# Optimization experiments

Hardware: AMD Instinct MI355X
Metric: run time of the kernel (lower is better)

Reference implementation:

```python
import jax, jax.numpy as jnp
import numpy as np

EPS = 1e-8

def _fft_unit_proj(x):
    # Project each vector to unit magnitude in the Fourier domain (norm_kv=True).
    f = jnp.fft.fft(x, axis=-1)
    return jnp.real(jnp.fft.ifft(f / (jnp.abs(f) + EPS), axis=-1))

def _hrr_key_value_query(k, v, q, causal=True):
    # k, v, q: [B, S, D]
    k = _fft_unit_proj(k)
    v = _fft_unit_proj(v)
    # bind: circular convolution of key and value
    kv = jnp.real(jnp.fft.ifft(jnp.fft.fft(k, axis=-1) * jnp.fft.fft(v, axis=-1), axis=-1))
    # causal associative memory: running sum of bound pairs along sequence
    if causal:
        mem = jnp.cumsum(kv, axis=1)
    else:
        mem = jnp.broadcast_to(jnp.sum(kv, axis=1, keepdims=True), kv.shape)
    # unbind: circular correlation of memory with query
    out = jnp.real(jnp.fft.ifft(jnp.conj(jnp.fft.fft(q, axis=-1)) * jnp.fft.fft(mem, axis=-1), axis=-1))
    return out


def setup_inputs() -> dict:
    key = jax.random.key(0)
    ks = jax.random.split(key, 8)
    B, S, D = 2, 4096, 2048
    sc = 1.0 / np.sqrt(D).astype(np.float32)
    return {
        "hidden_states": jax.random.normal(ks[0], (B, S, D), jnp.float32),
        "base_output": jax.random.normal(ks[1], (B, S, D), jnp.float32),
        "Wq": jax.random.normal(ks[2], (D, D), jnp.float32) * sc,
        "bq": jnp.zeros((D,), jnp.float32),
        "Wk": jax.random.normal(ks[3], (D, D), jnp.float32) * sc,
        "bk": jnp.zeros((D,), jnp.float32),
        "Wv": jax.random.normal(ks[4], (D, D), jnp.float32) * sc,
        "bv": jnp.zeros((D,), jnp.float32),
        "gate": jax.random.normal(ks[5], (1,), jnp.float32) * 0.1,
    }


def reference(hidden_states, base_output, Wq, bq, Wk, bk, Wv, bv, gate):
    # Adapter q/k/v projections (nn.Linear uses y = x @ W.T + b)
    q = jnp.einsum('bsd,ed->bse', hidden_states, Wq) + bq
    k = jnp.einsum('bsd,ed->bse', hidden_states, Wk) + bk
    v = jnp.einsum('bsd,ed->bse', hidden_states, Wv) + bv
    adapter = _hrr_key_value_query(k, v, q, causal=True)
    return base_output + gate * adapter
```

## Files before the change

kernel.cpp:

```cpp
#include <hip/hip_runtime.h>
#include <math.h>

constexpr int D_DIM  = 2048;
constexpr int HALF_D = 1024;
constexpr int B_DIM  = 2;
constexpr int S_DIM  = 4096;
constexpr int NROW   = B_DIM * S_DIM;
constexpr int NCHUNK = 64;
constexpr int CHLEN  = S_DIM / NCHUNK;
constexpr float EPS_ = 1e-8f;

typedef __attribute__((ext_vector_type(8))) short  short8;
typedef __attribute__((ext_vector_type(8))) unsigned short ushort8;
typedef __attribute__((ext_vector_type(4))) float  f32x4;

__device__ __forceinline__ float2 mkf2(float x, float y){ float2 r; r.x=x; r.y=y; return r; }
__device__ __forceinline__ float2 cmulf(float2 a, float2 b){
  return mkf2(fmaf(a.x, b.x, -a.y*b.y), fmaf(a.x, b.y, a.y*b.x));
}
__device__ __forceinline__ unsigned short f2bf(float x){
  unsigned u = __float_as_uint(x);
  u += 0x7fff + ((u >> 16) & 1);
  return (unsigned short)(u >> 16);
}
__device__ __forceinline__ float bf2f(unsigned short h){
  return __uint_as_float(((unsigned)h) << 16);
}

__global__ __launch_bounds__(256)
void cvt_f32_bf16(const float* __restrict__ in, unsigned short* __restrict__ out, int n8)
{
  int i = blockIdx.x * 256 + threadIdx.x;
  if (i >= n8) return;
  const float4* p = (const float4*)in + (size_t)i * 2;
  float4 a = p[0], b = p[1];
  ushort8 o;
  o[0]=f2bf(a.x); o[1]=f2bf(a.y); o[2]=f2bf(a.z); o[3]=f2bf(a.w);
  o[4]=f2bf(b.x); o[5]=f2bf(b.y); o[6]=f2bf(b.z); o[7]=f2bf(b.w);
  *(ushort8*)(out + (size_t)i * 8) = o;
}

__global__ __launch_bounds__(512, 2)
void gemm_fused(const unsigned short* __restrict__ A,
                const unsigned short* __restrict__ Wc,
                const float* __restrict__ bq, const float* __restrict__ bk,
                const float* __restrict__ bv,
                float* __restrict__ qout, float* __restrict__ kout,
                unsigned short* __restrict__ vout)
{
  constexpr int K = 2048, NT = K / 32;
  __shared__ unsigned short lds[49152];
  const int tid  = threadIdx.x;
  const int wid  = tid >> 6, lane = tid & 63;
  const int wr   = wid >> 2, wc = wid & 3;

  int bid = blockIdx.x;
  int sw  = (bid & 7) * 96 + (bid >> 3);
  const int bm = (sw / 24) * 256, bn = (sw % 24) * 256;

  const int srow = tid >> 2;
  const int skc  = ((tid & 3) ^ ((tid >> 3) & 3)) * 8;
  const unsigned short* Ag = A  + (size_t)(bm + srow) * K + skc;
  const unsigned short* Bg = Wc + (size_t)(bn + srow) * K + skc;

  unsigned short* Abase = lds;
  unsigned short* Bbase = lds + 24576;
  const int stoff = wid * 512;

  const int fr  = lane & 15;
  const int sig = ((lane >> 4) ^ ((lane >> 1) & 3)) * 8;
  const int aro = (wr * 128 + fr) * 32 + sig;
  const int bro = (wc * 64 + fr) * 32 + sig;

  auto stA = [&](int kt, int b, int r) {
    __builtin_amdgcn_global_load_lds(
      (const __attribute__((address_space(1))) void*)(Ag + (size_t)r * 128 * K + kt * 32),
      (__attribute__((address_space(3))) void*)(Abase + b * 8192 + r * 4096 + stoff),
      16, 0, 0);
  };
  auto stB = [&](int kt, int b, int r) {
    __builtin_amdgcn_global_load_lds(
      (const __attribute__((address_space(1))) void*)(Bg + (size_t)r * 128 * K + kt * 32),
      (__attribute__((address_space(3))) void*)(Bbase + b * 8192 + r * 4096 + stoff),
      16, 0, 0);
  };

  f32x4 acc[8][4];
#pragma unroll
  for (int i = 0; i < 8; ++i)
#pragma unroll
    for (int j = 0; j < 4; ++j) acc[i][j] = (f32x4){0.f, 0.f, 0.f, 0.f};

  stA(0, 0, 0); stA(0, 0, 1); stB(0, 0, 0); stB(0, 0, 1);
  stA(1, 1, 0); stA(1, 1, 1); stB(1, 1, 0); stB(1, 1, 1);
  asm volatile("s_waitcnt vmcnt(4)" ::: "memory");
  __builtin_amdgcn_s_barrier();
  __builtin_amdgcn_sched_barrier(0);

  int c = 0;
#pragma unroll 1
  for (int kt = 0; kt < NT; ++kt) {
    const unsigned short* Ab = Abase + c * 8192;
    const unsigned short* Bb = Bbase + c * 8192;
    int nb = c + 2; if (nb >= 3) nb -= 3;

    if (kt < NT - 2) { stA(kt + 2, nb, 0); stA(kt + 2, nb, 1); }
    short8 af0[4], bfr[4];
#pragma unroll
    for (int i = 0; i < 4; ++i) af0[i] = *(const short8*)(Ab + aro + i * 512);
#pragma unroll
    for (int j = 0; j < 4; ++j) bfr[j] = *(const short8*)(Bb + bro + j * 512);
    __builtin_amdgcn_s_setprio(1);
#pragma unroll
    for (int i = 0; i < 4; ++i)
#pragma unroll
      for (int j = 0; j < 4; ++j)
        acc[i][j] = __builtin_amdgcn_mfma_f32_16x16x32_bf16(af0[i], bfr[j], acc[i][j], 0, 0, 0);
    __builtin_amdgcn_s_setprio(0);

    if (kt < NT - 2) { stB(kt + 2, nb, 0); stB(kt + 2, nb, 1); }
    short8 af1[4];
#pragma unroll
    for (int i = 0; i < 4; ++i) af1[i] = *(const short8*)(Ab + aro + 2048 + i * 512);
    __builtin_amdgcn_s_setprio(1);
#pragma unroll
    for (int i = 0; i < 4; ++i)
#pragma unroll
      for (int j = 0; j < 4; ++j)
        acc[4 + i][j] = __builtin_amdgcn_mfma_f32_16x16x32_bf16(af1[i], bfr[j], acc[4 + i][j], 0, 0, 0);
    __builtin_amdgcn_s_setprio(0);

    if (kt < NT - 1) {
      if (kt < NT - 2) asm volatile("s_waitcnt vmcnt(4)" ::: "memory");
      else             asm volatile("s_waitcnt vmcnt(0)" ::: "memory");
      __builtin_amdgcn_s_barrier();
      __builtin_amdgcn_sched_barrier(0);
    }
    c = (c == 2) ? 0 : c + 1;
  }

  const int seg = bn >> 11;
  const float* bp = (seg == 0) ? bq : (seg == 1) ? bk : bv;
  float bias_j[4];
#pragma unroll
  for (int j = 0; j < 4; ++j)
    bias_j[j] = bp[(bn + wc * 64 + j * 16 + fr) & 2047];
  const int er = (lane >> 4) * 4;
#pragma unroll
  for (int I = 0; I < 8; ++I) {
    int row = bm + wr * 128 + (I >> 2) * 64 + (I & 3) * 16 + er;
#pragma unroll
    for (int j = 0; j < 4; ++j) {
      int col = (bn + wc * 64 + j * 16 + fr) & 2047;
#pragma unroll
      for (int r = 0; r < 4; ++r) {
        float val = acc[I][j][r] + bias_j[j];
        if (seg == 2)
          vout[(size_t)(row + r) * 2048 + col] = f2bf(val);
        else if (seg == 1)
          kout[(size_t)(row + r) * 2048 + col] = val;
        else
          qout[(size_t)(row + r) * 2048 + col] = val;
      }
    }
  }
}

__device__ __forceinline__ int XS(int i){ return i ^ (((i >> 5) ^ (i >> 10)) & 31); }
__device__ __forceinline__ int TS(int i){ return i ^ ((i >> 5) & 31); }

__device__ __forceinline__ float2 mulmi(float2 w){ return mkf2(w.y, -w.x); }
__device__ __forceinline__ float2 mulw8(float2 w){
  const float c = 0.70710678118654752f;
  return mkf2(c * (w.x + w.y), c * (w.y - w.x));
}
__device__ __forceinline__ void bfly(float2& a, float2& b, float2 w){
  float2 v = cmulf(w, b);
  b = mkf2(a.x - v.x, a.y - v.y);
  a = mkf2(a.x + v.x, a.y + v.y);
}
__device__ __forceinline__ void bflyc(float2& a, float2& b, float2 w){
  float2 d = mkf2(a.x - b.x, a.y - b.y);
  a = mkf2(a.x + b.x, a.y + b.y);
  b = mkf2(fmaf(d.x, w.x, d.y * w.y), fmaf(d.y, w.x, -d.x * w.y));
}

__device__ __forceinline__ void fwd8(float2 e[8], float2 wA, float2 wB0, float2 wC0){
  bfly(e[0], e[1], wA); bfly(e[2], e[3], wA); bfly(e[4], e[5], wA); bfly(e[6], e[7], wA);
  float2 wB1 = mulmi(wB0);
  bfly(e[0], e[2], wB0); bfly(e[1], e[3], wB1); bfly(e[4], e[6], wB0); bfly(e[5], e[7], wB1);
  float2 wC1 = mulw8(wC0), wC2 = mulmi(wC0), wC3 = mulmi(wC1);
  bfly(e[0], e[4], wC0); bfly(e[1], e[5], wC1); bfly(e[2], e[6], wC2); bfly(e[3], e[7], wC3);
}
__device__ __forceinline__ void inv8(float2 e[8], float2 wA, float2 wB0, float2 wC0){
  float2 wC1 = mulw8(wC0), wC2 = mulmi(wC0), wC3 = mulmi(wC1);
  bflyc(e[0], e[4], wC0); bflyc(e[1], e[5], wC1); bflyc(e[2], e[6], wC2); bflyc(e[3], e[7], wC3);
  float2 wB1 = mulmi(wB0);
  bflyc(e[0], e[2], wB0); bflyc(e[1], e[3], wB1); bflyc(e[4], e[6], wB0); bflyc(e[5], e[7], wB1);
  bflyc(e[0], e[1], wA); bflyc(e[2], e[3], wA); bflyc(e[4], e[5], wA); bflyc(e[6], e[7], wA);
}

__device__ __forceinline__ float2 twld(const float* twr, const float* twi, int i){
  int s = TS(i);
  return mkf2(twr[s], twi[s]);
}

__device__ void fft_fwd(float2* X, const float* twr, const float* twi, int t)
{
  const float2 one = mkf2(1.f, 0.f);
  {
    int b = 8 * t;
    float2 e[8];
#pragma unroll
    for (int r = 0; r < 8; ++r) e[r] = X[XS(b + r)];
    fwd8(e, one, one, one);
#pragma unroll
    for (int r = 0; r < 8; ++r) X[XS(b + r)] = e[r];
  }
  __syncthreads();
  {
    int u = t >> 5, b = 64 * (t & 31) + u;
    float2 e[8];
#pragma unroll
    for (int r = 0; r < 8; ++r) e[r] = X[XS(b + 8 * r)];
    fwd8(e, twld(twr,twi,128*u), twld(twr,twi,64*u), twld(twr,twi,32*u));
#pragma unroll
    for (int r = 0; r < 8; ++r) X[XS(b + 8 * r)] = e[r];
  }
  __syncthreads();
  {
    int u = t & 63, b = 512 * (t >> 6) + u;
    float2 e[8];
#pragma unroll
    for (int r = 0; r < 8; ++r) e[r] = X[XS(b + 64 * r)];
    fwd8(e, twld(twr,twi,16*u), twld(twr,twi,8*u), twld(twr,twi,4*u));
#pragma unroll
    for (int r = 0; r < 8; ++r) X[XS(b + 64 * r)] = e[r];
  }
  __syncthreads();
#pragma unroll
  for (int h = 0; h < 2; ++h) {
    int u = t + 256 * h;
    float2 f[4];
#pragma unroll
    for (int r = 0; r < 4; ++r) f[r] = X[XS(u + 512 * r)];
    float2 wA = twld(twr,twi,2*u), wB0 = twld(twr,twi,u), wB1 = mulmi(wB0);
    bfly(f[0], f[1], wA);  bfly(f[2], f[3], wA);
    bfly(f[0], f[2], wB0); bfly(f[1], f[3], wB1);
#pragma unroll
    for (int r = 0; r < 4; ++r) X[XS(u + 512 * r)] = f[r];
  }
  __syncthreads();
}

__device__ void fft_inv(float2* X, const float* twr, const float* twi, int t)
{
  const float2 one = mkf2(1.f, 0.f);
#pragma unroll
  for (int h = 0; h < 2; ++h) {
    int u = t + 256 * h;
    float2 f[4];
#pragma unroll
    for (int r = 0; r < 4; ++r) f[r] = X[XS(u + 512 * r)];
    float2 wA = twld(twr,twi,2*u), wB0 = twld(twr,twi,u), wB1 = mulmi(wB0);
    bflyc(f[0], f[2], wB0); bflyc(f[1], f[3], wB1);
    bflyc(f[0], f[1], wA);  bflyc(f[2], f[3], wA);
#pragma unroll
    for (int r = 0; r < 4; ++r) X[XS(u + 512 * r)] = f[r];
  }
  __syncthreads();
  {
    int u = t & 63, b = 512 * (t >> 6) + u;
    float2 e[8];
#pragma unroll
    for (int r = 0; r < 8; ++r) e[r] = X[XS(b + 64 * r)];
    inv8(e, twld(twr,twi,16*u), twld(twr,twi,8*u), twld(twr,twi,4*u));
#pragma unroll
    for (int r = 0; r < 8; ++r) X[XS(b + 64 * r)] = e[r];
  }
  __syncthreads();
  {
    int u = t >> 5, b = 64 * (t & 31) + u;
    float2 e[8];
#pragma unroll
    for (int r = 0; r < 8; ++r) e[r] = X[XS(b + 8 * r)];
    inv8(e, twld(twr,twi,128*u), twld(twr,twi,64*u), twld(twr,twi,32*u));
#pragma unroll
    for (int r = 0; r < 8; ++r) X[XS(b + 8 * r)] = e[r];
  }
  __syncthreads();
  {
    int b = 8 * t;
    float2 e[8];
#pragma unroll
    for (int r = 0; r < 8; ++r) e[r] = X[XS(b + r)];
    inv8(e, one, one, one);
#pragma unroll
    for (int r = 0; r < 8; ++r) X[XS(b + r)] = e[r];
  }
  __syncthreads();
}

__global__ __launch_bounds__(256)
void twiddle_init(float2* __restrict__ twg)
{
  int i = blockIdx.x * 256 + threadIdx.x;
  if (i < HALF_D) {
    float sv, cv;
    sincosf(-6.283185307179586f * (float)i / (float)D_DIM, &sv, &cv);
    twg[i] = mkf2(cv, sv);
  }
}

__global__ __launch_bounds__(256)
void fftkv_kernel(float* __restrict__ kbuf, const unsigned short* __restrict__ vbuf,
                  const float2* __restrict__ twg)
{
  __shared__ float2 X[D_DIM];
  __shared__ float twr[HALF_D], twi[HALF_D];
  const int t = threadIdx.x;
  const size_t row = blockIdx.x;
  const float* krow = kbuf + row * D_DIM;
  const unsigned short* vrow = vbuf + row * D_DIM;

  for (int i = t; i < HALF_D; i += 256) {
    float2 w = twg[i]; int s = TS(i); twr[s] = w.x; twi[s] = w.y;
  }
  for (int i = t; i < D_DIM; i += 256) {
    int p = __brev((unsigned)i) >> 21;
    X[XS(p)] = mkf2(krow[i], bf2f(vrow[i]));
  }
  __syncthreads();
  fft_fwd(X, twr, twi, t);

  float2* outp = (float2*)(kbuf + row * D_DIM);
  for (int d = t; d < HALF_D; d += 256) {
    float2 p;
    if (d == 0) {
      float2 z0 = X[XS(0)], zn = X[XS(HALF_D)];
      float k0 = z0.x, v0 = z0.y, kn = zn.x, vn = zn.y;
      float p0 = (k0 / (fabsf(k0) + EPS_)) * (v0 / (fabsf(v0) + EPS_));
      float pn = (kn / (fabsf(kn) + EPS_)) * (vn / (fabsf(vn) + EPS_));
      p = mkf2(p0, pn);
    } else {
      float2 A = X[XS(d)];
      float2 Bc = X[XS(D_DIM - d)];
      float2 Bj = mkf2(Bc.x, -Bc.y);
      float2 Fk = mkf2(0.5f * (A.x + Bj.x), 0.5f * (A.y + Bj.y));
      float2 tt = mkf2(0.5f * (A.x - Bj.x), 0.5f * (A.y - Bj.y));
      float2 Fv = mkf2(tt.y, -tt.x);
      float sa = 1.f / (sqrtf(Fk.x*Fk.x + Fk.y*Fk.y) + EPS_);
      float sb = 1.f / (sqrtf(Fv.x*Fv.x + Fv.y*Fv.y) + EPS_);
      p = cmulf(Fk, Fv);
      float sc = sa * sb;
      p.x *= sc; p.y *= sc;
    }
    outp[d] = p;
  }
}

__global__ __launch_bounds__(256)
void scan_partial(const float2* __restrict__ kv, float2* __restrict__ part)
{
  int gid = blockIdx.x * 256 + threadIdx.x;
  int d = gid & (HALF_D - 1);
  int chunk = (gid >> 10) & (NCHUNK - 1);
  int b = gid >> 16;
  const float2* p = kv + ((size_t)(b * S_DIM + chunk * CHLEN) * HALF_D) + d;
  float2 acc = mkf2(0.f, 0.f);
  for (int s = 0; s < CHLEN; ++s) {
    float2 v = p[(size_t)s * HALF_D];
    acc.x += v.x; acc.y += v.y;
  }
  part[gid] = acc;
}

__global__ __launch_bounds__(256)
void scan_offsets(float2* __restrict__ part)
{
  int gid = blockIdx.x * 256 + threadIdx.x;
  int d = gid & (HALF_D - 1);
  int b = gid >> 10;
  float2* p = part + (size_t)b * (NCHUNK * HALF_D) + d;
  float2 acc = mkf2(0.f, 0.f);
  for (int c = 0; c < NCHUNK; ++c) {
    float2 v = p[(size_t)c * HALF_D];
    p[(size_t)c * HALF_D] = acc;
    acc.x += v.x; acc.y += v.y;
  }
}

__global__ __launch_bounds__(256)
void scan_apply(float2* __restrict__ kv, const float2* __restrict__ part)
{
  int gid = blockIdx.x * 256 + threadIdx.x;
  int d = gid & (HALF_D - 1);
  int chunk = (gid >> 10) & (NCHUNK - 1);
  int b = gid >> 16;
  float2* p = kv + ((size_t)(b * S_DIM + chunk * CHLEN) * HALF_D) + d;
  float2 acc = part[gid];
  for (int s = 0; s < CHLEN; ++s) {
    float2 v = p[(size_t)s * HALF_D];
    acc.x += v.x; acc.y += v.y;
    p[(size_t)s * HALF_D] = acc;
  }
}

__global__ __launch_bounds__(256)
void final_kernel(float* __restrict__ qo, const float2* __restrict__ mem,
                  const float* __restrict__ base, const float* __restrict__ gate,
                  const float2* __restrict__ twg)
{
  __shared__ float2 X[D_DIM];
  __shared__ float twr[HALF_D], twi[HALF_D];
  const int t = threadIdx.x;
  const size_t row = blockIdx.x;
  float* qrow = qo + row * D_DIM;
  const float2* mrow = mem + row * HALF_D;

  for (int i = t; i < HALF_D; i += 256) {
    float2 w = twg[i]; int s = TS(i); twr[s] = w.x; twi[s] = w.y;
  }
  for (int i = t; i < D_DIM; i += 256) {
    int p = __brev((unsigned)i) >> 21;
    X[XS(p)] = mkf2(qrow[i], 0.f);
  }
  __syncthreads();
  fft_fwd(X, twr, twi, t);

  for (int d = t; d < HALF_D; d += 256) {
    if (d == 0) {
      float2 fm = mrow[0];
      float2 f0 = X[XS(0)], f1 = X[XS(HALF_D)];
      X[XS(0)]      = mkf2(f0.x * fm.x, -f0.y * fm.x);
      X[XS(HALF_D)] = mkf2(f1.x * fm.y, -f1.y * fm.y);
    } else {
      float2 fm = mrow[d];
      float2 fq = X[XS(d)];
      X[XS(d)] = mkf2(fq.x*fm.x + fq.y*fm.y, fq.x*fm.y - fq.y*fm.x);
      float2 f2 = X[XS(D_DIM - d)];
      X[XS(D_DIM - d)] = mkf2(f2.x*fm.x - f2.y*fm.y, -f2.x*fm.y - f2.y*fm.x);
    }
  }
  __syncthreads();
  fft_inv(X, twr, twi, t);

  const float gv = gate[0] * (1.f / (float)D_DIM);
  const float* brow = base + row * D_DIM;
  for (int i = t; i < D_DIM; i += 256) {
    int p = __brev((unsigned)i) >> 21;
    qrow[i] = brow[i] + gv * X[XS(p)].x;
  }
}

extern "C" void kernel_launch(void* const* d_in, const int* in_sizes, int n_in,
                              void* d_out, int out_size, void* d_ws, size_t ws_size,
                              hipStream_t stream)
{
  const float* hs   = (const float*)d_in[0];
  const float* base = (const float*)d_in[1];
  const float* Wq   = (const float*)d_in[2];
  const float* bq   = (const float*)d_in[3];
  const float* Wk   = (const float*)d_in[4];
  const float* bk   = (const float*)d_in[5];
  const float* Wv   = (const float*)d_in[6];
  const float* bv   = (const float*)d_in[7];
  const float* gate = (const float*)d_in[8];
  float* out  = (float*)d_out;

  char* ws = (char*)d_ws;
  unsigned short* hsb = (unsigned short*)ws;
  unsigned short* wqb = (unsigned short*)(ws + 33554432);
  unsigned short* wkb = wqb + (size_t)D_DIM * D_DIM;
  unsigned short* wvb = wkb + (size_t)D_DIM * D_DIM;
  float*  kbuf = (float*)(ws + 58720256);
  unsigned short* vbuf = (unsigned short*)(ws + 58720256 + 67108864);
  float2* part = (float2*)(ws + 58720256 + 67108864 + 33554432);
  float2* twg  = (float2*)ws;

  {
    int n8 = (NROW * D_DIM) / 8;
    cvt_f32_bf16<<<n8 / 256, 256, 0, stream>>>(hs, hsb, n8);
    int w8 = (D_DIM * D_DIM) / 8;
    cvt_f32_bf16<<<w8 / 256, 256, 0, stream>>>(Wq, wqb, w8);
    cvt_f32_bf16<<<w8 / 256, 256, 0, stream>>>(Wk, wkb, w8);
    cvt_f32_bf16<<<w8 / 256, 256, 0, stream>>>(Wv, wvb, w8);
  }

  gemm_fused<<<768, 512, 0, stream>>>(hsb, wqb, bq, bk, bv, out, kbuf, vbuf);

  twiddle_init<<<4, 256, 0, stream>>>(twg);

  fftkv_kernel<<<NROW, 256, 0, stream>>>(kbuf, vbuf, twg);

  scan_partial<<<(B_DIM * NCHUNK * HALF_D) / 256, 256, 0, stream>>>(
      (const float2*)kbuf, part);
  scan_offsets<<<(B_DIM * HALF_D) / 256, 256, 0, stream>>>(part);
  scan_apply<<<(B_DIM * NCHUNK * HALF_D) / 256, 256, 0, stream>>>(
      (float2*)kbuf, part);

  final_kernel<<<NROW, 256, 0, stream>>>(out, (const float2*)kbuf, base, gate, twg);
}
```

Measured before the change: 438.3 us.

## Store K as bf16 interleaved with V and add intra-iteration GEMM barriers

The GEMM epilogue now writes K in bf16 instead of fp32, packed next to V in a single interleaved row buffer. The FFT kernel reads both halves from that one buffer and writes its spectrum back in place. This is meant to cut GEMM store traffic and FFT load traffic, at the cost of rounding K to bf16 before the unit-magnitude projection. The GEMM main loop also gains extra s_barrier and lgkmcnt waits around each MFMA phase, which tightens the schedule across waves but adds synchronisation.

New measurement: 433.3 us. About the same (-1.1%).

```diff
diff --git a/kernel.cpp b/kernel.cpp
--- a/kernel.cpp
+++ b/kernel.cpp
@@ -45,8 +45,7 @@
                 const unsigned short* __restrict__ Wc,
                 const float* __restrict__ bq, const float* __restrict__ bk,
                 const float* __restrict__ bv,
-                float* __restrict__ qout, float* __restrict__ kout,
-                unsigned short* __restrict__ vout)
+                float* __restrict__ qout, unsigned short* __restrict__ kvb)
 {
   constexpr int K = 2048, NT = K / 32;
   __shared__ unsigned short lds[49152];
@@ -103,13 +102,17 @@
     const unsigned short* Ab = Abase + c * 8192;
     const unsigned short* Bb = Bbase + c * 8192;
     int nb = c + 2; if (nb >= 3) nb -= 3;
-
-    if (kt < NT - 2) { stA(kt + 2, nb, 0); stA(kt + 2, nb, 1); }
+    const bool st = (kt < NT - 2);
+
+    if (st) { stA(kt + 2, nb, 0); stA(kt + 2, nb, 1); }
     short8 af0[4], bfr[4];
 #pragma unroll
     for (int i = 0; i < 4; ++i) af0[i] = *(const short8*)(Ab + aro + i * 512);
 #pragma unroll
     for (int j = 0; j < 4; ++j) bfr[j] = *(const short8*)(Bb + bro + j * 512);
+    __builtin_amdgcn_s_barrier();
+    asm volatile("s_waitcnt lgkmcnt(0)" ::: "memory");
+    __builtin_amdgcn_sched_barrier(0);
     __builtin_amdgcn_s_setprio(1);
 #pragma unroll
     for (int i = 0; i < 4; ++i)
@@ -117,11 +120,15 @@
       for (int j = 0; j < 4; ++j)
         acc[i][j] = __builtin_amdgcn_mfma_f32_16x16x32_bf16(af0[i], bfr[j], acc[i][j], 0, 0, 0);
     __builtin_amdgcn_s_setprio(0);
-
-    if (kt < NT - 2) { stB(kt + 2, nb, 0); stB(kt + 2, nb, 1); }
+    __builtin_amdgcn_s_barrier();
+
+    if (st) { stB(kt + 2, nb, 0); stB(kt + 2, nb, 1); }
     short8 af1[4];
 #pragma unroll
     for (int i = 0; i < 4; ++i) af1[i] = *(const short8*)(Ab + aro + 2048 + i * 512);
+    __builtin_amdgcn_s_barrier();
+    asm volatile("s_waitcnt lgkmcnt(0)" ::: "memory");
+    __builtin_amdgcn_sched_barrier(0);
     __builtin_amdgcn_s_setprio(1);
 #pragma unroll
     for (int i = 0; i < 4; ++i)
@@ -129,13 +136,9 @@
       for (int j = 0; j < 4; ++j)
         acc[4 + i][j] = __builtin_amdgcn_mfma_f32_16x16x32_bf16(af1[i], bfr[j], acc[4 + i][j], 0, 0, 0);
     __builtin_amdgcn_s_setprio(0);
-
-    if (kt < NT - 1) {
-      if (kt < NT - 2) asm volatile("s_waitcnt vmcnt(4)" ::: "memory");
-      else             asm volatile("s_waitcnt vmcnt(0)" ::: "memory");
-      __builtin_amdgcn_s_barrier();
-      __builtin_amdgcn_sched_barrier(0);
-    }
+    if (st)                 asm volatile("s_waitcnt vmcnt(4)" ::: "memory");
+    else if (kt == NT - 2)  asm volatile("s_waitcnt vmcnt(0)" ::: "memory");
+    __builtin_amdgcn_s_barrier();
     c = (c == 2) ? 0 : c + 1;
   }
 
@@ -146,21 +149,20 @@
   for (int j = 0; j < 4; ++j)
     bias_j[j] = bp[(bn + wc * 64 + j * 16 + fr) & 2047];
   const int er = (lane >> 4) * 4;
+  const int kvoff = (seg == 2) ? 2048 : 0;
 #pragma unroll
   for (int I = 0; I < 8; ++I) {
-    int row = bm + wr * 128 + (I >> 2) * 64 + (I & 3) * 16 + er;
+    int row = bm + wr * 128 + I * 16 + er;
 #pragma unroll
     for (int j = 0; j < 4; ++j) {
       int col = (bn + wc * 64 + j * 16 + fr) & 2047;
 #pragma unroll
       for (int r = 0; r < 4; ++r) {
         float val = acc[I][j][r] + bias_j[j];
-        if (seg == 2)
-          vout[(size_t)(row + r) * 2048 + col] = f2bf(val);
-        else if (seg == 1)
-          kout[(size_t)(row + r) * 2048 + col] = val;
+        if (seg == 0)
+          qout[(size_t)(row + r) * 2048 + col] = val;
         else
-          qout[(size_t)(row + r) * 2048 + col] = val;
+          kvb[(size_t)(row + r) * 4096 + kvoff + col] = f2bf(val);
       }
     }
   }
@@ -313,27 +315,25 @@
 }
 
 __global__ __launch_bounds__(256)
-void fftkv_kernel(float* __restrict__ kbuf, const unsigned short* __restrict__ vbuf,
-                  const float2* __restrict__ twg)
+void fftkv_kernel(unsigned short* __restrict__ kvb, const float2* __restrict__ twg)
 {
   __shared__ float2 X[D_DIM];
   __shared__ float twr[HALF_D], twi[HALF_D];
   const int t = threadIdx.x;
   const size_t row = blockIdx.x;
-  const float* krow = kbuf + row * D_DIM;
-  const unsigned short* vrow = vbuf + row * D_DIM;
+  const unsigned short* kvrow = kvb + row * 4096;
 
   for (int i = t; i < HALF_D; i += 256) {
     float2 w = twg[i]; int s = TS(i); twr[s] = w.x; twi[s] = w.y;
   }
   for (int i = t; i < D_DIM; i += 256) {
     int p = __brev((unsigned)i) >> 21;
-    X[XS(p)] = mkf2(krow[i], bf2f(vrow[i]));
+    X[XS(p)] = mkf2(bf2f(kvrow[i]), bf2f(kvrow[2048 + i]));
   }
   __syncthreads();
   fft_fwd(X, twr, twi, t);
 
-  float2* outp = (float2*)(kbuf + row * D_DIM);
+  float2* outp = (float2*)(kvb + row * 4096);
   for (int d = t; d < HALF_D; d += 256) {
     float2 p;
     if (d == 0) {
@@ -473,9 +473,8 @@
   unsigned short* wqb = (unsigned short*)(ws + 33554432);
   unsigned short* wkb = wqb + (size_t)D_DIM * D_DIM;
   unsigned short* wvb = wkb + (size_t)D_DIM * D_DIM;
-  float*  kbuf = (float*)(ws + 58720256);
-  unsigned short* vbuf = (unsigned short*)(ws + 58720256 + 67108864);
-  float2* part = (float2*)(ws + 58720256 + 67108864 + 33554432);
+  unsigned short* kvb = (unsigned short*)(ws + 58720256);
+  float2* part = (float2*)(ws + 58720256 + 67108864);
   float2* twg  = (float2*)ws;
 
   {
@@ -487,17 +486,17 @@
     cvt_f32_bf16<<<w8 / 256, 256, 0, stream>>>(Wv, wvb, w8);
   }
 
-  gemm_fused<<<768, 512, 0, stream>>>(hsb, wqb, bq, bk, bv, out, kbuf, vbuf);
+  gemm_fused<<<768, 512, 0, stream>>>(hsb, wqb, bq, bk, bv, out, kvb);
 
   twiddle_init<<<4, 256, 0, stream>>>(twg);
 
-  fftkv_kernel<<<NROW, 256, 0, stream>>>(kbuf, vbuf, twg);
+  fftkv_kernel<<<NROW, 256, 0, stream>>>(kvb, twg);
 
   scan_partial<<<(B_DIM * NCHUNK * HALF_D) / 256, 256, 0, stream>>>(
-      (const float2*)kbuf, part);
+      (const float2*)kvb, part);
   scan_offsets<<<(B_DIM * HALF_D) / 256, 256, 0, stream>>>(part);
   scan_apply<<<(B_DIM * NCHUNK * HALF_D) / 256, 256, 0, stream>>>(
-      (float2*)kbuf, part);
-
-  final_kernel<<<NROW, 256, 0, stream>>>(out, (const float2*)kbuf, base, gate, twg);
-}
+      (float2*)kvb, part);
+
+  final_kernel<<<NROW, 256, 0, stream>>>(out, (const float2*)kvb, base, gate, twg);
+}
```
